# Kernel optimization log

Measured on AMD Instinct MI355X. Metric: run time of the kernel, lower is better.

The kernel has to match this reference:

```python
import jax, jax.numpy as jnp
import numpy as np

DIM, HEADS, HID, L = 256, 8, 1024, 17
DI, DS, DTR = 2 * DIM, 4, DIM // 16  # mamba: d_inner, d_state, dt_rank
B = 4096
HOP = np.array([0, 1, 4, 7, 2, 5, 8, 3, 6, 9, 11, 14, 10, 12, 15, 13, 16])
GRAPH = np.array([0, 1, 4, 7, 2, 5, 8, 3, 6, 9, 12, 10, 13, 15, 11, 14, 16])
# Human3.6M 17-joint skeleton, symmetric-normalized adjacency with self loops
_EDGES = [(0,1),(1,2),(2,3),(0,4),(4,5),(5,6),(0,7),(7,8),(8,9),(9,10),(8,11),(11,12),(12,13),(8,14),(14,15),(15,16)]
_A = np.eye(L, dtype=np.float32)
for i, j in _EDGES:
    _A[i, j] = _A[j, i] = 1.0
_d = _A.sum(1)
A_HAT = jnp.asarray(_A / np.sqrt(np.outer(_d, _d)))


def ln(x, g, b):
    m = x.mean(-1, keepdims=True)
    v = ((x - m) ** 2).mean(-1, keepdims=True)
    return (x - m) * jax.lax.rsqrt(v + 1e-5) * g + b


def mamba(u, in_proj_w, conv_w, conv_b, x_proj_w, dt_proj_w, dt_proj_b, A_log, Dp, out_proj_w):
    # u: [B,L,DIM]
    xz = u @ in_proj_w                      # [B,L,2*DI]
    xm, z = jnp.split(xz, 2, axis=-1)
    xm = jax.nn.silu(xm * conv_w + conv_b)  # depthwise conv, kernel=1
    dbl = xm @ x_proj_w                     # [B,L,DTR+2*DS]
    dt = jax.nn.softplus(dbl[..., :DTR] @ dt_proj_w + dt_proj_b)  # [B,L,DI]
    Bm = dbl[..., DTR:DTR + DS]             # [B,L,DS]
    Cm = dbl[..., DTR + DS:]                # [B,L,DS]
    A = -jnp.exp(A_log)                     # [DI,DS]
    dA = jnp.exp(dt[..., None] * A)                               # [B,L,DI,DS]
    dBx = dt[..., None] * Bm[:, :, None, :] * xm[..., None]       # [B,L,DI,DS]

    def step(h, inp):
        dA_t, dBx_t, C_t = inp
        h = dA_t * h + dBx_t
        y = jnp.einsum('bds,bs->bd', h, C_t)
        return h, y

    h0 = jnp.zeros((u.shape[0], DI, DS), u.dtype)
    _, ys = jax.lax.scan(step, h0, (dA.transpose(1, 0, 2, 3), dBx.transpose(1, 0, 2, 3), Cm.transpose(1, 0, 2)))
    y = ys.transpose(1, 0, 2) + Dp * xm
    y = y * jax.nn.silu(z)
    return y @ out_proj_w


def setup_inputs() -> dict:
    key = jax.random.key(0)
    ks = iter(jax.random.split(key, 32))
    r = lambda shape, s=0.02: jax.random.normal(next(ks), shape, jnp.float32) * s
    inp = {
        'x': jax.random.normal(next(ks), (B, L, DIM), jnp.float32),
        # GCN sub-block
        'gcn_ln_g': jnp.ones((DIM,)), 'gcn_ln_b': jnp.zeros((DIM,)),
        'gcn_w1': r((DIM, 2 * DIM)), 'gcn_b1': jnp.zeros((2 * DIM,)),
        'gcn_w2': r((2 * DIM, DIM)), 'gcn_b2': jnp.zeros((DIM,)),
        # SSM sub-block
        'bp_embed': r((1, 5, DIM)),
        'ssm_ln_g': jnp.ones((DIM,)), 'ssm_ln_b': jnp.zeros((DIM,)),
        'in_proj_w': r((DIM, 2 * DI)),
        'conv_w': jnp.ones((DI,)), 'conv_b': jnp.zeros((DI,)),
        'x_proj_w': r((DI, DTR + 2 * DS)),
        'dt_proj_w': r((DTR, DI)), 'dt_proj_b': jnp.zeros((DI,)),
        'A_log': jnp.log(jnp.broadcast_to(jnp.arange(1, DS + 1, dtype=jnp.float32), (DI, DS))),
        'Dp': jnp.ones((DI,)),
        'out_proj_w': r((DI, DIM)),
        # Transformer sub-block
        'ln1_g': jnp.ones((DIM,)), 'ln1_b': jnp.zeros((DIM,)),
        'qkv_w': r((DIM, 3 * DIM)),
        'attn_proj_w': r((DIM, DIM)), 'attn_proj_b': jnp.zeros((DIM,)),
        'ln2_g': jnp.ones((DIM,)), 'ln2_b': jnp.zeros((DIM,)),
        'mlp_w1': r((DIM, HID)), 'mlp_b1': jnp.zeros((HID,)),
        'mlp_w2': r((HID, DIM)), 'mlp_b2': jnp.zeros((DIM,)),
    }
    return inp


def reference(x, gcn_ln_g, gcn_ln_b, gcn_w1, gcn_b1, gcn_w2, gcn_b2,
              bp_embed, ssm_ln_g, ssm_ln_b, in_proj_w, conv_w, conv_b,
              x_proj_w, dt_proj_w, dt_proj_b, A_log, Dp, out_proj_w,
              ln1_g, ln1_b, qkv_w, attn_proj_w, attn_proj_b,
              ln2_g, ln2_b, mlp_w1, mlp_b1, mlp_w2, mlp_b2):
    # ---- GCN sub-block (2-layer graph conv over 17-joint skeleton) ----
    res = x
    h = ln(x, gcn_ln_g, gcn_ln_b)
    h = jnp.einsum('ij,bjd->bid', A_HAT, h) @ gcn_w1 + gcn_b1
    h = jax.nn.gelu(h)
    h = jnp.einsum('ij,bjd->bid', A_HAT, h) @ gcn_w2 + gcn_b2
    x = res + h  # Block residual
    # ---- PoseSSM sub-block ----
    res = x
    bp = bp_embed[0]  # [5,DIM]
    x_bpe = jnp.concatenate([bp[:3], bp[:3], bp[:3], bp[:1], bp[3:], bp[:1], bp[3:], bp[3:]], axis=0)  # [17,DIM]
    xs = x[:, HOP, :] + x_bpe
    xs = ln(xs, ssm_ln_g, ssm_ln_b)
    xs = mamba(xs, in_proj_w, conv_w, conv_b, x_proj_w, dt_proj_w, dt_proj_b, A_log, Dp, out_proj_w)
    xs = xs[:, GRAPH, :]
    x = res + xs   # residual inside PoseSSM_module
    x = x + res    # residual in Block
    # ---- Transformer sub-block ----
    res = x
    t = ln(x, ln1_g, ln1_b)
    qkv = (t @ qkv_w).reshape(t.shape[0], L, 3, HEADS, DIM // HEADS)
    q, k, v = qkv[:, :, 0], qkv[:, :, 1], qkv[:, :, 2]  # [B,L,H,dh]
    scale = (DIM // HEADS) ** -0.5
    att = jax.nn.softmax(jnp.einsum('bqhd,bkhd->bhqk', q, k) * scale, axis=-1)
    o = jnp.einsum('bhqk,bkhd->bqhd', att, v).reshape(t.shape[0], L, DIM)
    o = o @ attn_proj_w + attn_proj_b
    x1 = x + o
    m = ln(x1, ln2_g, ln2_b)
    m = jax.nn.gelu(m @ mlp_w1 + mlp_b1) @ mlp_w2 + mlp_b2
    x2 = x1 + m
    return x2 + res
```

## Files before the change

kernel.cpp:

```cpp
#include <hip/hip_runtime.h>
#include <hip/hip_bf16.h>
#include <math.h>


#define LSEQ 17
#define RS 256
#define TS 264
#define SS 520
#define SCS 40
#define VTS 56
#define NTHR 1024
#define NWAVE 16

typedef unsigned short u16;
typedef __attribute__((ext_vector_type(8))) short short8;
typedef __attribute__((ext_vector_type(4))) float f32x4;

__device__ __forceinline__ float b2f(u16 u) {
    union { unsigned int i; float f; } x; x.i = ((unsigned int)u) << 16; return x.f;
}
__device__ __forceinline__ u16 f2b(float f) {
    union { float f; unsigned int i; } x; x.f = f;
    unsigned int r = x.i + 0x7FFFu + ((x.i >> 16) & 1u);
    return (u16)(r >> 16);
}
__device__ __forceinline__ float gelu_t(float x) {
    float u = 1.5957691216057308f * (x + 0.044715f * x * x * x);
    return x / (1.0f + __expf(-u));
}
__device__ __forceinline__ float siluf(float x) { return x / (1.0f + __expf(-x)); }
__device__ __forceinline__ float softplusf(float x) {
    return (x > 20.0f) ? x : __logf(1.0f + __expf(x));
}

__device__ const int HOPA[17]   = {0,1,4,7,2,5,8,3,6,9,11,14,10,12,15,13,16};
__device__ const int GRAPHA[17] = {0,1,4,7,2,5,8,3,6,9,12,10,13,15,11,14,16};
__device__ const int BPEI[17]   = {0,1,2,0,1,2,0,1,2,0,3,4,0,3,4,3,4};

#define OFF_GCN_W1   0
#define OFF_GCN_W2   131072
#define OFF_INPROJ   262144
#define OFF_OUTPROJ  524288
#define OFF_QKV      655360
#define OFF_ATTNPROJ 851968
#define OFF_MLP_W1   917504
#define OFF_MLP_W2   1179648
#define OFF_XPROJ    1441792

#define SM_R    0
#define SM_AC   34816
#define SM_T1   52768
#define SM_W5   70720
#define SM_U    106080
#define SM_VT   127840
#define SMEM_BYTES 156512

struct Params {
    const float *x, *gcn_ln_g, *gcn_ln_b, *gcn_w1, *gcn_b1, *gcn_w2, *gcn_b2,
                *bp_embed, *ssm_ln_g, *ssm_ln_b, *in_proj_w, *conv_w, *conv_b,
                *x_proj_w, *dt_proj_w, *dt_proj_b, *A_log, *Dp, *out_proj_w,
                *ln1_g, *ln1_b, *qkv_w, *attn_proj_w, *attn_proj_b,
                *ln2_g, *ln2_b, *mlp_w1, *mlp_b1, *mlp_w2, *mlp_b2;
    const u16* wws;
    float* out;
};

__global__ __launch_bounds__(256) void prepack(Params P) {
    const int gid = blockIdx.x * 256 + threadIdx.x;
    const int cnt[9]  = {16384,16384,32768,16384,24576,8192,32768,32768,2048};
    const int Ns [9]  = {512,256,1024,256,768,256,1024,256,24};
    const int NPs[9]  = {512,256,1024,256,768,256,1024,256,32};
    const int offs[9] = {OFF_GCN_W1,OFF_GCN_W2,OFF_INPROJ,OFF_OUTPROJ,OFF_QKV,
                         OFF_ATTNPROJ,OFF_MLP_W1,OFF_MLP_W2,OFF_XPROJ};
    int e = 0, base = 0;
    while (e < 9 && gid >= base + cnt[e]) { base += cnt[e]; ++e; }
    if (e >= 9) return;
    const float* W;
    switch (e) {
        case 0: W = P.gcn_w1; break;      case 1: W = P.gcn_w2; break;
        case 2: W = P.in_proj_w; break;   case 3: W = P.out_proj_w; break;
        case 4: W = P.qkv_w; break;       case 5: W = P.attn_proj_w; break;
        case 6: W = P.mlp_w1; break;      case 7: W = P.mlp_w2; break;
        default: W = P.x_proj_w; break;
    }
    const int local = gid - base;
    const int lane = local & 63, frag = local >> 6;
    const int NT = NPs[e] >> 4;
    const int nt = frag % NT, kc = frag / NT;
    const int n = nt * 16 + (lane & 15);
    const int kbase = kc * 32 + (lane >> 4) * 8;
    u16 v[8];
    #pragma unroll
    for (int j = 0; j < 8; ++j)
        v[j] = (n < Ns[e]) ? f2b(W[(size_t)(kbase + j) * Ns[e] + n]) : (u16)0;
    u16* dst = (u16*)P.wws + offs[e] + ((size_t)frag * 64 + lane) * 8;
    *(short8*)dst = *(short8*)v;
}

template <int KT>
__device__ __forceinline__ void mfmaAcc3(f32x4 acc[3],
        const u16* __restrict__ act, int ldin,
        const u16* __restrict__ wbase, int NT, int nt0, int ntcnt, int kc0) {
    const int lane = threadIdx.x & 63, wv = threadIdx.x >> 6;
    const int m = lane & 15, quad = lane >> 4;
    const bool v2 = (m < 2);
    const int ntl = wv;
    if (ntl >= ntcnt) return;
    for (int kc = 0; kc < KT; ++kc) {
        const int ko = kc * 32 + quad * 8;
        short8 a0 = *(const short8*)(act + m * ldin + ko);
        short8 a1 = *(const short8*)(act + (16 + m) * ldin + ko);
        short8 a2 = {0,0,0,0,0,0,0,0};
        if (v2) a2 = *(const short8*)(act + (32 + m) * ldin + ko);
        const short8 b = *(const short8*)(wbase +
            ((size_t)((kc0 + kc) * NT + nt0 + ntl) * 64 + lane) * 8);
        acc[0] = __builtin_amdgcn_mfma_f32_16x16x32_bf16(a0, b, acc[0], 0, 0, 0);
        acc[1] = __builtin_amdgcn_mfma_f32_16x16x32_bf16(a1, b, acc[1], 0, 0, 0);
        acc[2] = __builtin_amdgcn_mfma_f32_16x16x32_bf16(a2, b, acc[2], 0, 0, 0);
    }
}

template <class Epi>
__device__ __forceinline__ void mfmaStore3(f32x4 acc[3], int ntcnt, Epi epi) {
    const int lane = threadIdx.x & 63, wv = threadIdx.x >> 6;
    const int col0 = lane & 15, quad = lane >> 4;
    const int ntl = wv;
    if (ntl >= ntcnt) return;
    const int cb = ntl * 16 + col0;
    #pragma unroll
    for (int r = 0; r < 4; ++r) epi(quad * 4 + r, cb, acc[0][r]);
    #pragma unroll
    for (int r = 0; r < 4; ++r) epi(16 + quad * 4 + r, cb, acc[1][r]);
    if (quad == 0) {
        epi(32, cb, acc[2][0]);
        epi(33, cb, acc[2][1]);
    }
}

template <int KT, class Epi>
__device__ __forceinline__ void gemm3(const u16* act, int ldin,
        const u16* wbase, int NT, int nt0, int ntcnt, Epi epi) {
    f32x4 acc[3];
    #pragma unroll
    for (int mt = 0; mt < 3; ++mt) acc[mt] = (f32x4){0.f,0.f,0.f,0.f};
    mfmaAcc3<KT>(acc, act, ldin, wbase, NT, nt0, ntcnt, 0);
    mfmaStore3(acc, ntcnt, epi);
}

__global__ __launch_bounds__(NTHR, 4) void fused_block(Params P) {
    extern __shared__ __align__(16) char smem[];
    float* R   = (float*)(smem + SM_R);
    u16*   AC  = (u16*)  (smem + SM_AC);
    u16*   T1  = (u16*)  (smem + SM_T1);
    u16*   W5  = (u16*)  (smem + SM_W5);
    float* Dbl = (float*)(smem + SM_U);
    u16*   SC  = (u16*)  (smem + SM_U);
    u16*   VT  = (u16*)  (smem + SM_VT);

    const int tid = threadIdx.x;
    const int lane = tid & 63, wv = tid >> 6;
    const float* __restrict__ xg = P.x + (size_t)blockIdx.x * (2 * LSEQ * 256);
    const u16* __restrict__ ws = P.wws;

    for (int i4 = tid; i4 < 34 * 64; i4 += NTHR) {
        int rr = i4 >> 6, d4 = (i4 & 63) * 4;
        f32x4 v = __builtin_nontemporal_load((const f32x4*)(xg + rr * 256 + d4));
        *(f32x4*)(R + rr * RS + d4) = v;
    }
    __syncthreads();

    auto ln34 = [&](auto ld, u16* dst, const float* g, const float* bb) {
        for (int rr = wv; rr < 34; rr += NWAVE) {
            float v[4], s = 0.f, s2 = 0.f;
            #pragma unroll
            for (int j = 0; j < 4; ++j) {
                v[j] = ld(rr, lane + 64 * j);
                s += v[j]; s2 += v[j] * v[j];
            }
            #pragma unroll
            for (int m = 1; m < 64; m <<= 1) {
                s  += __shfl_xor(s, m, 64);
                s2 += __shfl_xor(s2, m, 64);
            }
            float mean = s * (1.0f / 256.0f);
            float var  = s2 * (1.0f / 256.0f) - mean * mean;
            float rstd = rsqrtf(var + 1e-5f);
            #pragma unroll
            for (int j = 0; j < 4; ++j) {
                int d = lane + 64 * j;
                dst[rr * TS + d] = f2b((v[j] - mean) * rstd * g[d] + bb[d]);
            }
        }
    };
    auto gconvCols = [&](int width, auto ldf, auto stf) {
        for (int u = tid; u < 2 * width; u += NTHR) {
            int e = u / width, d = u - e * width;
            float c[17];
            #pragma unroll
            for (int j = 0; j < 17; ++j) c[j] = ldf(e, j, d);
            float o[17];
            o[0]  = 0.25f*c[0] + 0.28867513f*(c[1]+c[4]+c[7]);
            o[1]  = 0.28867513f*c[0] + 0.33333334f*(c[1]+c[2]);
            o[2]  = 0.33333334f*(c[1]+c[2]) + 0.40824829f*c[3];
            o[3]  = 0.40824829f*c[2] + 0.5f*c[3];
            o[4]  = 0.28867513f*c[0] + 0.33333334f*(c[4]+c[5]);
            o[5]  = 0.33333334f*(c[4]+c[5]) + 0.40824829f*c[6];
            o[6]  = 0.40824829f*c[5] + 0.5f*c[6];
            o[7]  = 0.28867513f*c[0] + 0.33333334f*c[7] + 0.25819889f*c[8];
            o[8]  = 0.25819889f*(c[7]+c[9]+c[11]+c[14]) + 0.2f*c[8];
            o[9]  = 0.25819889f*c[8] + 0.33333334f*c[9] + 0.40824829f*c[10];
            o[10] = 0.40824829f*c[9] + 0.5f*c[10];
            o[11] = 0.25819889f*c[8] + 0.33333334f*(c[11]+c[12]);
            o[12] = 0.33333334f*(c[11]+c[12]) + 0.40824829f*c[13];
            o[13] = 0.40824829f*c[12] + 0.5f*c[13];
            o[14] = 0.25819889f*c[8] + 0.33333334f*(c[14]+c[15]);
            o[15] = 0.33333334f*(c[14]+c[15]) + 0.40824829f*c[16];
            o[16] = 0.40824829f*c[15] + 0.5f*c[16];
            #pragma unroll
            for (int i = 0; i < 17; ++i) stf(e, i, d, o[i]);
        }
    };

    ln34([&](int rr, int d) { return R[rr * RS + d]; }, AC, P.gcn_ln_g, P.gcn_ln_b);
    __syncthreads();
    gconvCols(256,
        [&](int e, int j, int d) { return b2f(AC[(e * 17 + j) * TS + d]); },
        [&](int e, int i, int d, float v) { AC[(e * 17 + i) * TS + d] = f2b(v); });
    __syncthreads();
    gemm3<8>(AC, TS, ws + OFF_GCN_W1, 32, 0, 16,
        [&](int rr, int c, float v) { W5[rr * SS + c] = f2b(gelu_t(v + P.gcn_b1[c])); });
    gemm3<8>(AC, TS, ws + OFF_GCN_W1, 32, 16, 16,
        [&](int rr, int c, float v) { W5[rr * SS + 256 + c] = f2b(gelu_t(v + P.gcn_b1[256 + c])); });
    __syncthreads();
    gemm3<16>(W5, SS, ws + OFF_GCN_W2, 16, 0, 16,
        [&](int rr, int c, float v) { AC[rr * TS + c] = f2b(v); });
    __syncthreads();
    gconvCols(256,
        [&](int e, int j, int d) { return b2f(AC[(e * 17 + j) * TS + d]); },
        [&](int e, int i, int d, float v) { R[(e * 17 + i) * RS + d] += v + P.gcn_b2[d]; });
    __syncthreads();

    for (int i = tid; i < 34 * 256; i += NTHR) {
        int rr = i >> 8, d = i & 255;
        int e = (rr >= 17), l = rr - e * 17;
        AC[rr * TS + d] = f2b(R[(e * 17 + HOPA[l]) * RS + d] + P.bp_embed[BPEI[l] * 256 + d]);
    }
    __syncthreads();
    ln34([&](int rr, int d) { return b2f(AC[rr * TS + d]); }, T1, P.ssm_ln_g, P.ssm_ln_b);
    __syncthreads();
    gemm3<8>(T1, TS, ws + OFF_INPROJ, 64, 0, 16,
        [&](int rr, int c, float v) { W5[rr * SS + c] = f2b(siluf(v * P.conv_w[c] + P.conv_b[c])); });
    gemm3<8>(T1, TS, ws + OFF_INPROJ, 64, 16, 16,
        [&](int rr, int c, float v) { W5[rr * SS + 256 + c] = f2b(siluf(v * P.conv_w[256 + c] + P.conv_b[256 + c])); });
    __syncthreads();
    gemm3<16>(W5, SS, ws + OFF_XPROJ, 2, 0, 2,
        [&](int rr, int c, float v) { if (c < 24) Dbl[rr * 24 + c] = v; });
    __syncthreads();
    {
        const int e = tid >> 9, d = tid & 511;
        const int rb = e * LSEQ;
        float wdt[16];
        #pragma unroll
        for (int r = 0; r < 16; ++r) wdt[r] = P.dt_proj_w[r * 512 + d];
        const float dtb = P.dt_proj_b[d];
        float Ar[4];
        #pragma unroll
        for (int s = 0; s < 4; ++s) Ar[s] = -__expf(P.A_log[d * 4 + s]);
        const float Dpd = P.Dp[d];
        float h0 = 0.f, h1 = 0.f, h2 = 0.f, h3 = 0.f;
        for (int t = 0; t < LSEQ; ++t) {
            const float* Dv = Dbl + (rb + t) * 24;
            float a = dtb;
            #pragma unroll
            for (int r = 0; r < 16; ++r) a += Dv[r] * wdt[r];
            float dt_ = softplusf(a);
            float xm = b2f(W5[(rb + t) * SS + d]);
            float p = dt_ * xm;
            h0 = __expf(dt_ * Ar[0]) * h0 + p * Dv[16];
            h1 = __expf(dt_ * Ar[1]) * h1 + p * Dv[17];
            h2 = __expf(dt_ * Ar[2]) * h2 + p * Dv[18];
            h3 = __expf(dt_ * Ar[3]) * h3 + p * Dv[19];
            float y = h0 * Dv[20] + h1 * Dv[21] + h2 * Dv[22] + h3 * Dv[23] + Dpd * xm;
            W5[(rb + t) * SS + d] = f2b(y);
        }
    }
    __syncthreads();
    gemm3<8>(T1, TS, ws + OFF_INPROJ, 64, 32, 16,
        [&](int rr, int c, float v) {
            float y = b2f(W5[rr * SS + c]);
            W5[rr * SS + c] = f2b(y * siluf(v));
        });
    gemm3<8>(T1, TS, ws + OFF_INPROJ, 64, 48, 16,
        [&](int rr, int c, float v) {
            float y = b2f(W5[rr * SS + 256 + c]);
            W5[rr * SS + 256 + c] = f2b(y * siluf(v));
        });
    __syncthreads();
    gemm3<16>(W5, SS, ws + OFF_OUTPROJ, 16, 0, 16,
        [&](int rr, int c, float v) { AC[rr * TS + c] = f2b(v); });
    __syncthreads();
    for (int i = tid; i < 34 * 256; i += NTHR) {
        int rr = i >> 8, d = i & 255;
        int e = (rr >= 17), l = rr - e * 17;
        R[rr * RS + d] = 2.0f * R[rr * RS + d] + b2f(AC[(e * 17 + GRAPHA[l]) * TS + d]);
    }
    __syncthreads();

    ln34([&](int rr, int d) { return R[rr * RS + d]; }, AC, P.ln1_g, P.ln1_b);
    for (int i = tid; i < (256 * VTS) / 2; i += NTHR)
        ((unsigned int*)VT)[i] = 0u;
    __syncthreads();
    gemm3<8>(AC, TS, ws + OFF_QKV, 48, 0, 16,
        [&](int rr, int c, float v) { T1[rr * TS + c] = f2b(v); });
    gemm3<8>(AC, TS, ws + OFF_QKV, 48, 16, 16,
        [&](int rr, int c, float v) { W5[rr * SS + c] = f2b(v); });
    gemm3<8>(AC, TS, ws + OFF_QKV, 48, 32, 16,
        [&](int rr, int c, float v) {
            int e2 = (rr >= 17), t = rr - e2 * 17;
            VT[c * VTS + e2 * 24 + t] = f2b(v);
        });
    __syncthreads();
    {
        const int e = wv >> 3, h = wv & 7, m16 = lane & 15, quad = lane >> 4;
        const int rb = e * LSEQ;
        const u16* qb = T1 + rb * TS + h * 32 + quad * 8;
        const u16* kb = W5 + rb * SS + h * 32 + quad * 8;
        short8 qa0 = *(const short8*)(qb + m16 * TS);
        short8 ka0 = *(const short8*)(kb + m16 * SS);
        short8 qa1 = {0,0,0,0,0,0,0,0}, ka1 = {0,0,0,0,0,0,0,0};
        if (m16 == 0) {
            qa1 = *(const short8*)(qb + 16 * TS);
            ka1 = *(const short8*)(kb + 16 * SS);
        }
        f32x4 s00 = {0.f,0.f,0.f,0.f}, s01 = s00, s10 = s00, s11 = s00;
        s00 = __builtin_amdgcn_mfma_f32_16x16x32_bf16(qa0, ka0, s00, 0, 0, 0);
        s01 = __builtin_amdgcn_mfma_f32_16x16x32_bf16(qa0, ka1, s01, 0, 0, 0);
        s10 = __builtin_amdgcn_mfma_f32_16x16x32_bf16(qa1, ka0, s10, 0, 0, 0);
        s11 = __builtin_amdgcn_mfma_f32_16x16x32_bf16(qa1, ka1, s11, 0, 0, 0);
        const float sc = 0.17677669529663687f;
        u16* sh = SC + wv * 17 * SCS;
        #pragma unroll
        for (int r = 0; r < 4; ++r) {
            int i = quad * 4 + r;
            sh[i * SCS + m16]      = f2b(s00[r] * sc);
            sh[i * SCS + 16 + m16] = f2b(s01[r] * sc);
        }
        if (quad == 0) {
            sh[16 * SCS + m16]      = f2b(s10[0] * sc);
            sh[16 * SCS + 16 + m16] = f2b(s11[0] * sc);
        }
    }
    __syncthreads();
    if (tid < 272) {
        u16* row = SC + tid * SCS;
        float e[17], mx = -3.0e38f, sum = 0.f;
        #pragma unroll
        for (int j = 0; j < 17; ++j) mx = fmaxf(mx, b2f(row[j]));
        #pragma unroll
        for (int j = 0; j < 17; ++j) { e[j] = __expf(b2f(row[j]) - mx); sum += e[j]; }
        float inv = 1.0f / sum;
        #pragma unroll
        for (int j = 0; j < 17; ++j) row[j] = f2b(e[j] * inv);
    }
    __syncthreads();
    {
        const int e = wv >> 3, h = wv & 7, m16 = lane & 15, quad = lane >> 4;
        const int rb = e * LSEQ;
        const u16* sh = SC + wv * 17 * SCS + quad * 8;
        short8 pa0 = *(const short8*)(sh + m16 * SCS);
        short8 pa1 = {0,0,0,0,0,0,0,0};
        if (m16 == 0) pa1 = *(const short8*)(sh + 16 * SCS);
        #pragma unroll
        for (int nt = 0; nt < 2; ++nt) {
            const int n = h * 32 + nt * 16 + m16;
            short8 vb = {0,0,0,0,0,0,0,0};
            if (quad < 3) vb = *(const short8*)(VT + n * VTS + e * 24 + quad * 8);
            f32x4 o0 = {0.f,0.f,0.f,0.f}, o1 = o0;
            o0 = __builtin_amdgcn_mfma_f32_16x16x32_bf16(pa0, vb, o0, 0, 0, 0);
            o1 = __builtin_amdgcn_mfma_f32_16x16x32_bf16(pa1, vb, o1, 0, 0, 0);
            #pragma unroll
            for (int r = 0; r < 4; ++r) {
                int i = quad * 4 + r;
                AC[(rb + i) * TS + h * 32 + nt * 16 + m16] = f2b(o0[r]);
            }
            if (quad == 0)
                AC[(rb + 16) * TS + h * 32 + nt * 16 + m16] = f2b(o1[0]);
        }
    }
    __syncthreads();
    gemm3<8>(AC, TS, ws + OFF_ATTNPROJ, 16, 0, 16,
        [&](int rr, int c, float v) { T1[rr * TS + c] = f2b(v + P.attn_proj_b[c]); });
    __syncthreads();

    ln34([&](int rr, int d) { return R[rr * RS + d] + b2f(T1[rr * TS + d]); },
         AC, P.ln2_g, P.ln2_b);
    __syncthreads();
    {
        f32x4 accO[3];
        #pragma unroll
        for (int mt = 0; mt < 3; ++mt) accO[mt] = (f32x4){0.f,0.f,0.f,0.f};
        #pragma unroll
        for (int half = 0; half < 2; ++half) {
            #pragma unroll
            for (int sub = 0; sub < 2; ++sub) {
                const int base = half * 512 + sub * 256;
                gemm3<8>(AC, TS, ws + OFF_MLP_W1, 64, half * 32 + sub * 16, 16,
                    [&](int rr, int c, float v) {
                        W5[rr * SS + sub * 256 + c] = f2b(gelu_t(v + P.mlp_b1[base + c]));
                    });
            }
            __syncthreads();
            mfmaAcc3<16>(accO, W5, SS, ws + OFF_MLP_W2, 16, 0, 16, half * 16);
            __syncthreads();
        }
        float* outg = P.out + (size_t)blockIdx.x * (2 * LSEQ * 256);
        mfmaStore3(accO, 16, [&](int rr, int c, float v) {
            float r = v + P.mlp_b2[c] + 2.0f * R[rr * RS + c] + b2f(T1[rr * TS + c]);
            __builtin_nontemporal_store(r, outg + rr * 256 + c);
        });
    }
}

extern "C" void kernel_launch(void* const* d_in, const int* in_sizes, int n_in,
                              void* d_out, int out_size, void* d_ws, size_t ws_size,
                              hipStream_t stream) {
    (void)in_sizes; (void)n_in; (void)ws_size; (void)out_size;
    Params P;
    P.x           = (const float*)d_in[0];
    P.gcn_ln_g    = (const float*)d_in[1];
    P.gcn_ln_b    = (const float*)d_in[2];
    P.gcn_w1      = (const float*)d_in[3];
    P.gcn_b1      = (const float*)d_in[4];
    P.gcn_w2      = (const float*)d_in[5];
    P.gcn_b2      = (const float*)d_in[6];
    P.bp_embed    = (const float*)d_in[7];
    P.ssm_ln_g    = (const float*)d_in[8];
    P.ssm_ln_b    = (const float*)d_in[9];
    P.in_proj_w   = (const float*)d_in[10];
    P.conv_w      = (const float*)d_in[11];
    P.conv_b      = (const float*)d_in[12];
    P.x_proj_w    = (const float*)d_in[13];
    P.dt_proj_w   = (const float*)d_in[14];
    P.dt_proj_b   = (const float*)d_in[15];
    P.A_log       = (const float*)d_in[16];
    P.Dp          = (const float*)d_in[17];
    P.out_proj_w  = (const float*)d_in[18];
    P.ln1_g       = (const float*)d_in[19];
    P.ln1_b       = (const float*)d_in[20];
    P.qkv_w       = (const float*)d_in[21];
    P.attn_proj_w = (const float*)d_in[22];
    P.attn_proj_b = (const float*)d_in[23];
    P.ln2_g       = (const float*)d_in[24];
    P.ln2_b       = (const float*)d_in[25];
    P.mlp_w1      = (const float*)d_in[26];
    P.mlp_b1      = (const float*)d_in[27];
    P.mlp_w2      = (const float*)d_in[28];
    P.mlp_b2      = (const float*)d_in[29];
    P.wws         = (const u16*)d_ws;
    P.out         = (float*)d_out;
    static int smem_set = 0;
    if (!smem_set) {
        hipFuncSetAttribute(reinterpret_cast<const void*>(fused_block),
                            hipFuncAttributeMaxDynamicSharedMemorySize, SMEM_BYTES);
        smem_set = 1;
    }
    hipLaunchKernelGGL(prepack, dim3(712), dim3(256), 0, stream, P);
    hipLaunchKernelGGL(fused_block, dim3(2048), dim3(NTHR), SMEM_BYTES, stream, P);
}
```

Before: 779.6 us.

## Fuse layernorms with adjacent elementwise passes and split graph-conv rows across threads

Fuses the input load with the first layernorm, the HOP gather plus body-part embedding add with the SSM layernorm, and the residual-plus-GRAPH gather with the ln1 layernorm. This removes several full-block barriers and intermediate LDS round trips. Layernorm now gives each lane four contiguous columns and writes them as one vectorized store. The graph convolution now uses all 1024 threads, each half computing part of the output rows, at the cost of every thread loading all 17 inputs. Buffer roles for Q and the layernorm output are swapped so the fused path can write into T1.

```diff
diff --git a/kernel.cpp b/kernel.cpp
--- a/kernel.cpp
+++ b/kernel.cpp
@@ -14,6 +14,7 @@
 
 typedef unsigned short u16;
 typedef __attribute__((ext_vector_type(8))) short short8;
+typedef __attribute__((ext_vector_type(4))) short short4v;
 typedef __attribute__((ext_vector_type(4))) float f32x4;
 
 __device__ __forceinline__ float b2f(u16 u) {
@@ -69,7 +70,7 @@
     const int gid = blockIdx.x * 256 + threadIdx.x;
     const int cnt[9]  = {16384,16384,32768,16384,24576,8192,32768,32768,2048};
     const int Ns [9]  = {512,256,1024,256,768,256,1024,256,24};
-    const int NPs[9]  = {512,256,1024,256,768,256,1024,256,32};
+    const int NPs[9] = {512,256,1024,256,768,256,1024,256,32};
     const int offs[9] = {OFF_GCN_W1,OFF_GCN_W2,OFF_INPROJ,OFF_OUTPROJ,OFF_QKV,
                          OFF_ATTNPROJ,OFF_MLP_W1,OFF_MLP_W2,OFF_XPROJ};
     int e = 0, base = 0;
@@ -162,68 +163,73 @@
     const float* __restrict__ xg = P.x + (size_t)blockIdx.x * (2 * LSEQ * 256);
     const u16* __restrict__ ws = P.wws;
 
-    for (int i4 = tid; i4 < 34 * 64; i4 += NTHR) {
-        int rr = i4 >> 6, d4 = (i4 & 63) * 4;
-        f32x4 v = __builtin_nontemporal_load((const f32x4*)(xg + rr * 256 + d4));
-        *(f32x4*)(R + rr * RS + d4) = v;
-    }
-    __syncthreads();
-
+    auto lnStore = [&](float v[4], u16* dst, int rr, int d0,
+                       const float* g, const float* bb) {
+        float s = v[0] + v[1] + v[2] + v[3];
+        float s2 = v[0]*v[0] + v[1]*v[1] + v[2]*v[2] + v[3]*v[3];
+        #pragma unroll
+        for (int m = 1; m < 64; m <<= 1) {
+            s  += __shfl_xor(s, m, 64);
+            s2 += __shfl_xor(s2, m, 64);
+        }
+        float mean = s * (1.0f / 256.0f);
+        float var  = s2 * (1.0f / 256.0f) - mean * mean;
+        float rstd = rsqrtf(var + 1e-5f);
+        u16 o[4];
+        #pragma unroll
+        for (int j = 0; j < 4; ++j)
+            o[j] = f2b((v[j] - mean) * rstd * g[d0 + j] + bb[d0 + j]);
+        *(short4v*)(dst + rr * TS + d0) = *(short4v*)o;
+    };
     auto ln34 = [&](auto ld, u16* dst, const float* g, const float* bb) {
+        const int d0 = lane * 4;
         for (int rr = wv; rr < 34; rr += NWAVE) {
-            float v[4], s = 0.f, s2 = 0.f;
-            #pragma unroll
-            for (int j = 0; j < 4; ++j) {
-                v[j] = ld(rr, lane + 64 * j);
-                s += v[j]; s2 += v[j] * v[j];
-            }
-            #pragma unroll
-            for (int m = 1; m < 64; m <<= 1) {
-                s  += __shfl_xor(s, m, 64);
-                s2 += __shfl_xor(s2, m, 64);
-            }
-            float mean = s * (1.0f / 256.0f);
-            float var  = s2 * (1.0f / 256.0f) - mean * mean;
-            float rstd = rsqrtf(var + 1e-5f);
-            #pragma unroll
-            for (int j = 0; j < 4; ++j) {
-                int d = lane + 64 * j;
-                dst[rr * TS + d] = f2b((v[j] - mean) * rstd * g[d] + bb[d]);
-            }
+            float v[4];
+            #pragma unroll
+            for (int j = 0; j < 4; ++j) v[j] = ld(rr, d0 + j);
+            lnStore(v, dst, rr, d0, g, bb);
         }
     };
-    auto gconvCols = [&](int width, auto ldf, auto stf) {
-        for (int u = tid; u < 2 * width; u += NTHR) {
-            int e = u / width, d = u - e * width;
-            float c[17];
-            #pragma unroll
-            for (int j = 0; j < 17; ++j) c[j] = ldf(e, j, d);
-            float o[17];
-            o[0]  = 0.25f*c[0] + 0.28867513f*(c[1]+c[4]+c[7]);
-            o[1]  = 0.28867513f*c[0] + 0.33333334f*(c[1]+c[2]);
-            o[2]  = 0.33333334f*(c[1]+c[2]) + 0.40824829f*c[3];
-            o[3]  = 0.40824829f*c[2] + 0.5f*c[3];
-            o[4]  = 0.28867513f*c[0] + 0.33333334f*(c[4]+c[5]);
-            o[5]  = 0.33333334f*(c[4]+c[5]) + 0.40824829f*c[6];
-            o[6]  = 0.40824829f*c[5] + 0.5f*c[6];
-            o[7]  = 0.28867513f*c[0] + 0.33333334f*c[7] + 0.25819889f*c[8];
-            o[8]  = 0.25819889f*(c[7]+c[9]+c[11]+c[14]) + 0.2f*c[8];
-            o[9]  = 0.25819889f*c[8] + 0.33333334f*c[9] + 0.40824829f*c[10];
-            o[10] = 0.40824829f*c[9] + 0.5f*c[10];
-            o[11] = 0.25819889f*c[8] + 0.33333334f*(c[11]+c[12]);
-            o[12] = 0.33333334f*(c[11]+c[12]) + 0.40824829f*c[13];
-            o[13] = 0.40824829f*c[12] + 0.5f*c[13];
-            o[14] = 0.25819889f*c[8] + 0.33333334f*(c[14]+c[15]);
-            o[15] = 0.33333334f*(c[14]+c[15]) + 0.40824829f*c[16];
-            o[16] = 0.40824829f*c[15] + 0.5f*c[16];
-            #pragma unroll
-            for (int i = 0; i < 17; ++i) stf(e, i, d, o[i]);
+    auto gconvCols = [&](auto ldf, auto stf) {
+        const int u = tid & 511, half = tid >> 9;
+        const int e = u >> 8, d = u & 255;
+        float c[17];
+        #pragma unroll
+        for (int j = 0; j < 17; ++j) c[j] = ldf(e, j, d);
+        if (half == 0) {
+            stf(e, 0, d, 0.25f*c[0] + 0.28867513f*(c[1]+c[4]+c[7]));
+            stf(e, 1, d, 0.28867513f*c[0] + 0.33333334f*(c[1]+c[2]));
+            stf(e, 2, d, 0.33333334f*(c[1]+c[2]) + 0.40824829f*c[3]);
+            stf(e, 3, d, 0.40824829f*c[2] + 0.5f*c[3]);
+            stf(e, 4, d, 0.28867513f*c[0] + 0.33333334f*(c[4]+c[5]));
+            stf(e, 5, d, 0.33333334f*(c[4]+c[5]) + 0.40824829f*c[6]);
+            stf(e, 6, d, 0.40824829f*c[5] + 0.5f*c[6]);
+            stf(e, 7, d, 0.28867513f*c[0] + 0.33333334f*c[7] + 0.25819889f*c[8]);
+            stf(e, 8, d, 0.25819889f*(c[7]+c[9]+c[11]+c[14]) + 0.2f*c[8]);
+        } else {
+            stf(e, 9, d, 0.25819889f*c[8] + 0.33333334f*c[9] + 0.40824829f*c[10]);
+            stf(e,10, d, 0.40824829f*c[9] + 0.5f*c[10]);
+            stf(e,11, d, 0.25819889f*c[8] + 0.33333334f*(c[11]+c[12]));
+            stf(e,12, d, 0.33333334f*(c[11]+c[12]) + 0.40824829f*c[13]);
+            stf(e,13, d, 0.40824829f*c[12] + 0.5f*c[13]);
+            stf(e,14, d, 0.25819889f*c[8] + 0.33333334f*(c[14]+c[15]));
+            stf(e,15, d, 0.33333334f*(c[14]+c[15]) + 0.40824829f*c[16]);
+            stf(e,16, d, 0.40824829f*c[15] + 0.5f*c[16]);
         }
     };
 
-    ln34([&](int rr, int d) { return R[rr * RS + d]; }, AC, P.gcn_ln_g, P.gcn_ln_b);
-    __syncthreads();
-    gconvCols(256,
+    {
+        const int d0 = lane * 4;
+        for (int rr = wv; rr < 34; rr += NWAVE) {
+            f32x4 x4 = __builtin_nontemporal_load((const f32x4*)(xg + rr * 256 + d0));
+            *(f32x4*)(R + rr * RS + d0) = x4;
+            float v[4] = {x4[0], x4[1], x4[2], x4[3]};
+            lnStore(v, AC, rr, d0, P.gcn_ln_g, P.gcn_ln_b);
+        }
+    }
+    __syncthreads();
+
+    gconvCols(
         [&](int e, int j, int d) { return b2f(AC[(e * 17 + j) * TS + d]); },
         [&](int e, int i, int d, float v) { AC[(e * 17 + i) * TS + d] = f2b(v); });
     __syncthreads();
@@ -235,18 +241,23 @@
     gemm3<16>(W5, SS, ws + OFF_GCN_W2, 16, 0, 16,
         [&](int rr, int c, float v) { AC[rr * TS + c] = f2b(v); });
     __syncthreads();
-    gconvCols(256,
+    gconvCols(
         [&](int e, int j, int d) { return b2f(AC[(e * 17 + j) * TS + d]); },
         [&](int e, int i, int d, float v) { R[(e * 17 + i) * RS + d] += v + P.gcn_b2[d]; });
     __syncthreads();
 
-    for (int i = tid; i < 34 * 256; i += NTHR) {
-        int rr = i >> 8, d = i & 255;
-        int e = (rr >= 17), l = rr - e * 17;
-        AC[rr * TS + d] = f2b(R[(e * 17 + HOPA[l]) * RS + d] + P.bp_embed[BPEI[l] * 256 + d]);
-    }
-    __syncthreads();
-    ln34([&](int rr, int d) { return b2f(AC[rr * TS + d]); }, T1, P.ssm_ln_g, P.ssm_ln_b);
+    {
+        const int d0 = lane * 4;
+        for (int rr = wv; rr < 34; rr += NWAVE) {
+            int e = (rr >= 17), l = rr - e * 17;
+            const float* rs = R + (e * 17 + HOPA[l]) * RS;
+            const float* bp = P.bp_embed + BPEI[l] * 256;
+            float v[4];
+            #pragma unroll
+            for (int j = 0; j < 4; ++j) v[j] = rs[d0 + j] + bp[d0 + j];
+            lnStore(v, T1, rr, d0, P.ssm_ln_g, P.ssm_ln_b);
+        }
+    }
     __syncthreads();
     gemm3<8>(T1, TS, ws + OFF_INPROJ, 64, 0, 16,
         [&](int rr, int c, float v) { W5[rr * SS + c] = f2b(siluf(v * P.conv_w[c] + P.conv_b[c])); });
@@ -299,22 +310,28 @@
     gemm3<16>(W5, SS, ws + OFF_OUTPROJ, 16, 0, 16,
         [&](int rr, int c, float v) { AC[rr * TS + c] = f2b(v); });
     __syncthreads();
-    for (int i = tid; i < 34 * 256; i += NTHR) {
-        int rr = i >> 8, d = i & 255;
-        int e = (rr >= 17), l = rr - e * 17;
-        R[rr * RS + d] = 2.0f * R[rr * RS + d] + b2f(AC[(e * 17 + GRAPHA[l]) * TS + d]);
-    }
-    __syncthreads();
-
-    ln34([&](int rr, int d) { return R[rr * RS + d]; }, AC, P.ln1_g, P.ln1_b);
-    for (int i = tid; i < (256 * VTS) / 2; i += NTHR)
-        ((unsigned int*)VT)[i] = 0u;
-    __syncthreads();
-    gemm3<8>(AC, TS, ws + OFF_QKV, 48, 0, 16,
-        [&](int rr, int c, float v) { T1[rr * TS + c] = f2b(v); });
-    gemm3<8>(AC, TS, ws + OFF_QKV, 48, 16, 16,
+
+    {
+        const int d0 = lane * 4;
+        for (int rr = wv; rr < 34; rr += NWAVE) {
+            int e = (rr >= 17), l = rr - e * 17;
+            const u16* ms = AC + (e * 17 + GRAPHA[l]) * TS;
+            float* rrow = R + rr * RS;
+            float v[4];
+            #pragma unroll
+            for (int j = 0; j < 4; ++j) v[j] = 2.0f * rrow[d0 + j] + b2f(ms[d0 + j]);
+            *(f32x4*)(rrow + d0) = (f32x4){v[0], v[1], v[2], v[3]};
+            lnStore(v, T1, rr, d0, P.ln1_g, P.ln1_b);
+        }
+        for (int i = tid; i < (256 * VTS) / 2; i += NTHR)
+            ((unsigned int*)VT)[i] = 0u;
+    }
+    __syncthreads();
+    gemm3<8>(T1, TS, ws + OFF_QKV, 48, 0, 16,
+        [&](int rr, int c, float v) { AC[rr * TS + c] = f2b(v); });
+    gemm3<8>(T1, TS, ws + OFF_QKV, 48, 16, 16,
         [&](int rr, int c, float v) { W5[rr * SS + c] = f2b(v); });
-    gemm3<8>(AC, TS, ws + OFF_QKV, 48, 32, 16,
+    gemm3<8>(T1, TS, ws + OFF_QKV, 48, 32, 16,
         [&](int rr, int c, float v) {
             int e2 = (rr >= 17), t = rr - e2 * 17;
             VT[c * VTS + e2 * 24 + t] = f2b(v);
@@ -323,7 +340,7 @@
     {
         const int e = wv >> 3, h = wv & 7, m16 = lane & 15, quad = lane >> 4;
         const int rb = e * LSEQ;
-        const u16* qb = T1 + rb * TS + h * 32 + quad * 8;
+        const u16* qb = AC + rb * TS + h * 32 + quad * 8;
         const u16* kb = W5 + rb * SS + h * 32 + quad * 8;
         short8 qa0 = *(const short8*)(qb + m16 * TS);
         short8 ka0 = *(const short8*)(kb + m16 * SS);
```

New measurement: 744.3 us. -4.5%, faster.
